# Optimization experiments

Measured on AMD Instinct MI355X. Metric: run time of the kernel, lower is better.

Reference implementation:

```python
import jax, jax.numpy as jnp
import numpy as np

N_NODES = 50000
N_EDGES = 800000
F_IN = 128
HIDDEN = 128
F_OUT = 64
BN_EPS = 1e-5


def setup_inputs() -> dict:
    key = jax.random.key(0)
    ks = jax.random.split(key, 8)
    features = jax.random.normal(ks[0], (N_NODES, F_IN), dtype=jnp.float32)
    W1 = jax.random.normal(ks[1], (2 * F_IN, HIDDEN), dtype=jnp.float32) * 0.05
    b1 = jnp.zeros((HIDDEN,), dtype=jnp.float32)
    gamma = jnp.ones((HIDDEN,), dtype=jnp.float32)
    beta = jnp.zeros((HIDDEN,), dtype=jnp.float32)
    W2 = jax.random.normal(ks[2], (2 * HIDDEN, F_OUT), dtype=jnp.float32) * 0.05
    b2 = jnp.zeros((F_OUT,), dtype=jnp.float32)
    edge_vals = jax.random.uniform(ks[3], (N_EDGES,), dtype=jnp.float32)
    edge_src = jax.random.randint(ks[4], (N_EDGES,), 0, N_NODES, dtype=jnp.int32)
    edge_dst = jax.random.randint(ks[5], (N_EDGES,), 0, N_NODES, dtype=jnp.int32)
    return {"features": features, "W1": W1, "b1": b1, "gamma": gamma,
            "beta": beta, "W2": W2, "b2": b2, "edge_vals": edge_vals,
            "edge_src": edge_src, "edge_dst": edge_dst}


def _spmm(edge_vals, edge_src, edge_dst, x):
    # agg[i] = sum_{e: dst_e == i} w_e * x[src_e]   (sparse adjacency @ x)
    msgs = edge_vals[:, None] * x[edge_src]          # [E, d]
    return jax.ops.segment_sum(msgs, edge_dst, num_segments=N_NODES)


def _batchnorm(x, gamma, beta):
    # BatchNorm1d in training mode: batch stats, biased variance
    mean = jnp.mean(x, axis=0)
    var = jnp.mean(jnp.square(x - mean), axis=0)
    return gamma * (x - mean) * jax.lax.rsqrt(var + BN_EPS) + beta


def reference(features, W1, b1, gamma, beta, W2, b2, edge_vals, edge_src, edge_dst):
    # Layer 1: SpMM -> concat -> linear -> batchnorm -> relu  (dropout is a no-op, p=0)
    agg = _spmm(edge_vals, edge_src, edge_dst, features)     # [N, F_IN]
    s = jnp.concatenate([agg, features], axis=1)             # [N, 2*F_IN]
    h = s @ W1 + b1                                          # [N, HIDDEN]
    h = jax.nn.relu(_batchnorm(h, gamma, beta))
    # Layer 2: SpMM -> concat -> linear (identity act, no norm)
    agg2 = _spmm(edge_vals, edge_src, edge_dst, h)           # [N, HIDDEN]
    s2 = jnp.concatenate([agg2, h], axis=1)                  # [N, 2*HIDDEN]
    out = s2 @ W2 + b2                                       # [N, F_OUT]
    return out
```

## Files before the change

### kernel.cpp

```cpp
#include <hip/hip_runtime.h>

#define N_NODES 50000
#define N_EDGES 800000
#define F_IN    128
#define HID     128
#define F_OUT   64
#define BN_EPS  1e-5f

#define NRANGES 196
#define NCHUNKS 196
#define CHUNK   4096
#define CVT_BLOCKS 3125
#define PREPW_BLOCKS 24

typedef __bf16 bf16x8 __attribute__((ext_vector_type(8)));
typedef float  f32x4  __attribute__((ext_vector_type(4)));

static inline size_t align_up(size_t x, size_t a){ return (x + a - 1) / a * a; }

__device__ __forceinline__ float bflo(unsigned u){ return __uint_as_float(u << 16); }
__device__ __forceinline__ float bfhi(unsigned u){ return __uint_as_float(u & 0xffff0000u); }
__device__ __forceinline__ unsigned packbf(float a, float b){
  __bf16 ha = (__bf16)a, hb = (__bf16)b;
  unsigned short ua = __builtin_bit_cast(unsigned short, ha);
  unsigned short ub = __builtin_bit_cast(unsigned short, hb);
  return (unsigned)ua | ((unsigned)ub << 16);
}


__global__ __launch_bounds__(256) void k_setup(
    const int* __restrict__ dst, const float* __restrict__ X,
    const float* __restrict__ W1, const float* __restrict__ W2,
    int* __restrict__ Hcr, __bf16* __restrict__ Sx,
    __bf16* __restrict__ W1f, __bf16* __restrict__ W2f,
    float* __restrict__ bn_acc, int* __restrict__ bar){
  __shared__ int hist[NRANGES];
  int b = blockIdx.x, t = threadIdx.x;
  if(b < NCHUNKS){
    if(t < NRANGES) hist[t] = 0;
    __syncthreads();
    int e0 = b * CHUNK;
    #pragma unroll
    for(int k = 0; k < CHUNK / 256; k++){
      int e = e0 + k * 256 + t;
      if(e < N_EDGES) atomicAdd(&hist[dst[e] >> 8], 1);
    }
    __syncthreads();
    if(t < NRANGES) Hcr[b * NRANGES + t] = hist[t];
  } else if(b < NCHUNKS + CVT_BLOCKS){
    int bb = b - NCHUNKS;
    if(bb == 0){
      bn_acc[t] = 0.f;
      if(t < 2) bar[t] = 0;
    }
    int idx = bb * 256 + t;
    int n = idx >> 4;
    int c = (idx & 15) * 8;
    const float* xp = X + (size_t)n * F_IN + c;
    f32x4 x0 = *(const f32x4*)xp;
    f32x4 x1 = *(const f32x4*)(xp + 4);
    bf16x8 v;
    #pragma unroll
    for(int i = 0; i < 4; i++){ v[i] = (__bf16)x0[i]; v[4 + i] = (__bf16)x1[i]; }
    *(bf16x8*)(Sx + (size_t)n * 128 + c) = v;
  } else {
    int s = (b - NCHUNKS - CVT_BLOCKS) * 256 + t;
    if(s < 4096){
      int ks = s >> 9, rem = s & 511, nf = rem >> 6, l = rem & 63;
      int k = ks * 32 + (l >> 4) * 8, c = nf * 16 + (l & 15);
      bf16x8 v;
      #pragma unroll
      for(int i = 0; i < 8; i++) v[i] = (__bf16)W1[(size_t)(k + i) * HID + c];
      *(bf16x8*)(W1f + ((size_t)s << 3)) = v;
    } else {
      int q = s - 4096;
      int ks = q >> 9, rem = q & 511, nf = rem >> 6, l = rem & 63;
      int k = ks * 32 + (l >> 4) * 8, c = nf * 16 + (l & 15);
      bf16x8 v;
      #pragma unroll
      for(int i = 0; i < 8; i++){
        int kk = k + i;
        float val = (c < 64) ? W2[(size_t)kk * F_OUT + c]
                             : W2[(size_t)(HID + kk) * F_OUT + (c - 64)];
        v[i] = (__bf16)val;
      }
      *(bf16x8*)(W2f + ((size_t)q << 3)) = v;
    }
  }
}


__device__ __forceinline__ void grid_bar(int* bar, int n){
  __syncthreads();
  if(threadIdx.x == 0){
    __threadfence();
    atomicAdd(bar, 1);
    while(atomicAdd(bar, 0) < n){ }
    __threadfence();
  }
  __syncthreads();
}

__global__ __launch_bounds__(256) void k_csr(
    const int* __restrict__ dst, const int* __restrict__ src, const float* __restrict__ vals,
    int* __restrict__ Hcr, int* __restrict__ rtot, int2* __restrict__ staged,
    unsigned* __restrict__ epack, int* __restrict__ rp, int* __restrict__ bar){
  __shared__ int s[256];
  __shared__ int aux[256];
  __shared__ int begS, endS;
  const int b = blockIdx.x, t = threadIdx.x;

  {
    int v = (t < NCHUNKS) ? Hcr[t * NRANGES + b] : 0;
    s[t] = v;
    __syncthreads();
    for(int off = 1; off < 256; off <<= 1){
      int u = (t >= off) ? s[t - off] : 0;
      __syncthreads();
      s[t] += u;
      __syncthreads();
    }
    if(t < NCHUNKS) Hcr[t * NRANGES + b] = s[t] - v;
    if(t == NCHUNKS - 1) rtot[b] = s[t];
  }
  grid_bar(&bar[0], NRANGES);

  {
    int tv = (t < NRANGES) ? rtot[t] : 0;
    s[t] = tv;
    __syncthreads();
    for(int off = 1; off < 256; off <<= 1){
      int u = (t >= off) ? s[t - off] : 0;
      __syncthreads();
      s[t] += u;
      __syncthreads();
    }
    if(t < NRANGES) aux[t] = (s[t] - tv) + Hcr[b * NRANGES + t];
    __syncthreads();
    int e0 = b * CHUNK;
    #pragma unroll
    for(int k = 0; k < CHUNK / 256; k++){
      int e = e0 + k * 256 + t;
      if(e < N_EDGES){
        int d = dst[e];
        int pos = atomicAdd(&aux[d >> 8], 1);
        staged[pos] = make_int2(__float_as_int(vals[e]), src[e] | ((d & 255) << 16));
      }
    }
  }
  grid_bar(&bar[1], NRANGES);

  {
    int tv = (t < NRANGES) ? rtot[t] : 0;
    s[t] = tv;
    __syncthreads();
    for(int off = 1; off < 256; off <<= 1){
      int u = (t >= off) ? s[t - off] : 0;
      __syncthreads();
      s[t] += u;
      __syncthreads();
    }
    if(t == b){ begS = s[t] - tv; endS = s[t]; }
    aux[t] = 0;
    __syncthreads();
    int beg = begS, end = endS;
    for(int i = beg + t; i < end; i += 256)
      atomicAdd(&aux[(staged[i].y >> 16) & 255], 1);
    __syncthreads();
    int v = aux[t];
    s[t] = v;
    __syncthreads();
    for(int off = 1; off < 256; off <<= 1){
      int u = (t >= off) ? s[t - off] : 0;
      __syncthreads();
      s[t] += u;
      __syncthreads();
    }
    int excl = s[t] - v;
    int d = b * 256 + t;
    if(d < N_NODES) rp[d] = beg + excl;
    if(b == NRANGES - 1 && t == 0) rp[N_NODES] = N_EDGES;
    __syncthreads();
    aux[t] = beg + excl;
    __syncthreads();
    for(int i = beg + t; i < end; i += 256){
      int2 e = staged[i];
      int dl = (e.y >> 16) & 255;
      int p = atomicAdd(&aux[dl], 1);
      unsigned wb = (unsigned)__builtin_bit_cast(unsigned short, (__bf16)__int_as_float(e.x));
      epack[p] = (wb << 16) | (unsigned)(e.y & 0xffff);
    }
  }
}


__global__ __launch_bounds__(256) void k_spmm1(const __bf16* __restrict__ Sx,
    __bf16* __restrict__ Sa, const unsigned* __restrict__ epack, const int* __restrict__ rp){
  int w    = (int)((blockIdx.x * blockDim.x + threadIdx.x) >> 6);
  int lane = threadIdx.x & 63;
  if(w >= N_NODES) return;
  int beg = rp[w], end = rp[w + 1];
  float a0 = 0.f, a1 = 0.f;
  int e = beg;
  for(; e + 7 < end; e += 8){
    unsigned q0 = epack[e],     q1 = epack[e + 1], q2 = epack[e + 2], q3 = epack[e + 3];
    unsigned q4 = epack[e + 4], q5 = epack[e + 5], q6 = epack[e + 6], q7 = epack[e + 7];
    unsigned u0 = *(const unsigned*)(Sx + (size_t)(q0 & 0xffff) * 128 + lane * 2);
    unsigned u1 = *(const unsigned*)(Sx + (size_t)(q1 & 0xffff) * 128 + lane * 2);
    unsigned u2 = *(const unsigned*)(Sx + (size_t)(q2 & 0xffff) * 128 + lane * 2);
    unsigned u3 = *(const unsigned*)(Sx + (size_t)(q3 & 0xffff) * 128 + lane * 2);
    unsigned u4 = *(const unsigned*)(Sx + (size_t)(q4 & 0xffff) * 128 + lane * 2);
    unsigned u5 = *(const unsigned*)(Sx + (size_t)(q5 & 0xffff) * 128 + lane * 2);
    unsigned u6 = *(const unsigned*)(Sx + (size_t)(q6 & 0xffff) * 128 + lane * 2);
    unsigned u7 = *(const unsigned*)(Sx + (size_t)(q7 & 0xffff) * 128 + lane * 2);
    float w0 = bfhi(q0), w1 = bfhi(q1), w2 = bfhi(q2), w3 = bfhi(q3);
    float w4 = bfhi(q4), w5 = bfhi(q5), w6 = bfhi(q6), w7 = bfhi(q7);
    a0 = fmaf(w0, bflo(u0), a0); a1 = fmaf(w0, bfhi(u0), a1);
    a0 = fmaf(w1, bflo(u1), a0); a1 = fmaf(w1, bfhi(u1), a1);
    a0 = fmaf(w2, bflo(u2), a0); a1 = fmaf(w2, bfhi(u2), a1);
    a0 = fmaf(w3, bflo(u3), a0); a1 = fmaf(w3, bfhi(u3), a1);
    a0 = fmaf(w4, bflo(u4), a0); a1 = fmaf(w4, bfhi(u4), a1);
    a0 = fmaf(w5, bflo(u5), a0); a1 = fmaf(w5, bfhi(u5), a1);
    a0 = fmaf(w6, bflo(u6), a0); a1 = fmaf(w6, bfhi(u6), a1);
    a0 = fmaf(w7, bflo(u7), a0); a1 = fmaf(w7, bfhi(u7), a1);
  }
  for(; e + 3 < end; e += 4){
    unsigned q0 = epack[e], q1 = epack[e + 1], q2 = epack[e + 2], q3 = epack[e + 3];
    unsigned u0 = *(const unsigned*)(Sx + (size_t)(q0 & 0xffff) * 128 + lane * 2);
    unsigned u1 = *(const unsigned*)(Sx + (size_t)(q1 & 0xffff) * 128 + lane * 2);
    unsigned u2 = *(const unsigned*)(Sx + (size_t)(q2 & 0xffff) * 128 + lane * 2);
    unsigned u3 = *(const unsigned*)(Sx + (size_t)(q3 & 0xffff) * 128 + lane * 2);
    float w0 = bfhi(q0), w1 = bfhi(q1), w2 = bfhi(q2), w3 = bfhi(q3);
    a0 = fmaf(w0, bflo(u0), a0); a1 = fmaf(w0, bfhi(u0), a1);
    a0 = fmaf(w1, bflo(u1), a0); a1 = fmaf(w1, bfhi(u1), a1);
    a0 = fmaf(w2, bflo(u2), a0); a1 = fmaf(w2, bfhi(u2), a1);
    a0 = fmaf(w3, bflo(u3), a0); a1 = fmaf(w3, bfhi(u3), a1);
  }
  for(; e < end; e++){
    unsigned q = epack[e];
    float wt = bfhi(q);
    unsigned u = *(const unsigned*)(Sx + (size_t)(q & 0xffff) * 128 + lane * 2);
    a0 = fmaf(wt, bflo(u), a0); a1 = fmaf(wt, bfhi(u), a1);
  }
  *(unsigned*)(Sa + (size_t)w * 128 + lane * 2) = packbf(a0, a1);
}


__global__ __launch_bounds__(256) void k_gemm1(
    const __bf16* __restrict__ Sa, const __bf16* __restrict__ Sx,
    const __bf16* __restrict__ W1f, const float* __restrict__ b1,
    __bf16* __restrict__ hpre, float* __restrict__ bn_acc){
  __shared__ float bnred[2][256];
  const int tid = threadIdx.x;
  const int lane = tid & 63, wid = tid >> 6;
  const int wm = wid >> 1, wn = wid & 1;
  const int lr = lane & 15, lk = (lane >> 4) * 8;
  const int rbase = blockIdx.x * 64 + wm * 32 + lr;

  f32x4 acc[2][4];
  #pragma unroll
  for(int m = 0; m < 2; m++)
    #pragma unroll
    for(int n = 0; n < 4; n++) acc[m][n] = (f32x4){0.f, 0.f, 0.f, 0.f};

  for(int ks = 0; ks < 8; ks++){
    const __bf16* src = (ks < 4) ? Sa : Sx;
    const int kb = (ks & 3) * 32 + lk;
    bf16x8 a[2], b[4];
    #pragma unroll
    for(int m = 0; m < 2; m++){
      int r = rbase + m * 16; if(r > N_NODES - 1) r = N_NODES - 1;
      a[m] = *(const bf16x8*)(src + (size_t)r * 128 + kb);
    }
    #pragma unroll
    for(int n = 0; n < 4; n++)
      b[n] = *(const bf16x8*)(W1f + (((ks * 8 + wn * 4 + n) * 64 + lane) << 3));
    #pragma unroll
    for(int m = 0; m < 2; m++)
      #pragma unroll
      for(int n = 0; n < 4; n++)
        acc[m][n] = __builtin_amdgcn_mfma_f32_16x16x32_bf16(a[m], b[n], acc[m][n], 0, 0, 0);
  }

  #pragma unroll
  for(int n = 0; n < 4; n++){
    int gc = wn * 64 + n * 16 + lr;
    float bias = b1[gc];
    float ps = 0.f, pq = 0.f;
    #pragma unroll
    for(int m = 0; m < 2; m++){
      int gr0 = blockIdx.x * 64 + wm * 32 + m * 16 + (lane >> 4) * 4;
      #pragma unroll
      for(int i = 0; i < 4; i++){
        int r = gr0 + i;
        if(r < N_NODES){
          float h = acc[m][n][i] + bias;
          hpre[(size_t)r * HID + gc] = (__bf16)h;
          ps += h; pq += h * h;
        }
      }
    }
    ps += __shfl_xor(ps, 16); ps += __shfl_xor(ps, 32);
    pq += __shfl_xor(pq, 16); pq += __shfl_xor(pq, 32);
    if(lane < 16){
      bnred[wm][gc] = ps;
      bnred[wm][128 + gc] = pq;
    }
  }
  __syncthreads();
  atomicAdd(&bn_acc[tid], bnred[0][tid] + bnred[1][tid]);
}


__global__ __launch_bounds__(256) void k_gemm2(
    const __bf16* __restrict__ hpre, const __bf16* __restrict__ W2f,
    const float* __restrict__ b2, const float* __restrict__ bn_acc,
    const float* __restrict__ gamma, const float* __restrict__ beta,
    __bf16* __restrict__ y2b, float* __restrict__ out){
  __shared__ float s_scale[HID], s_shift[HID];
  const int tid = threadIdx.x;
  if(tid < HID){
    float mean = bn_acc[tid] / (float)N_NODES;
    float var  = bn_acc[HID + tid] / (float)N_NODES - mean * mean;
    float rs   = rsqrtf(var + BN_EPS);
    float sc   = gamma[tid] * rs;
    s_scale[tid] = sc;
    s_shift[tid] = beta[tid] - mean * sc;
  }
  const int lane = tid & 63, wid = tid >> 6;
  const int wm = wid >> 1, wn = wid & 1;
  const int lr = lane & 15, lk = (lane >> 4) * 8;
  const int rbase = blockIdx.x * 64 + wm * 32 + lr;

  f32x4 acc[2][4];
  #pragma unroll
  for(int m = 0; m < 2; m++)
    #pragma unroll
    for(int n = 0; n < 4; n++) acc[m][n] = (f32x4){0.f, 0.f, 0.f, 0.f};
  __syncthreads();

  for(int ks = 0; ks < 4; ks++){
    int k0 = ks * 32 + lk;
    f32x4 sc0 = *(const f32x4*)(s_scale + k0);
    f32x4 sc1 = *(const f32x4*)(s_scale + k0 + 4);
    f32x4 sh0 = *(const f32x4*)(s_shift + k0);
    f32x4 sh1 = *(const f32x4*)(s_shift + k0 + 4);
    bf16x8 a[2], b[4];
    #pragma unroll
    for(int m = 0; m < 2; m++){
      int r = rbase + m * 16; if(r > N_NODES - 1) r = N_NODES - 1;
      bf16x8 hv = *(const bf16x8*)(hpre + (size_t)r * HID + k0);
      bf16x8 af;
      #pragma unroll
      for(int i = 0; i < 4; i++){
        af[i]     = (__bf16)fmaxf(0.f, fmaf((float)hv[i],     sc0[i], sh0[i]));
        af[4 + i] = (__bf16)fmaxf(0.f, fmaf((float)hv[4 + i], sc1[i], sh1[i]));
      }
      a[m] = af;
    }
    #pragma unroll
    for(int n = 0; n < 4; n++)
      b[n] = *(const bf16x8*)(W2f + (((ks * 8 + wn * 4 + n) * 64 + lane) << 3));
    #pragma unroll
    for(int m = 0; m < 2; m++)
      #pragma unroll
      for(int n = 0; n < 4; n++)
        acc[m][n] = __builtin_amdgcn_mfma_f32_16x16x32_bf16(a[m], b[n], acc[m][n], 0, 0, 0);
  }

  #pragma unroll
  for(int n = 0; n < 4; n++){
    int c = n * 16 + lr;
    float bias = (wn == 1) ? b2[c] : 0.f;
    #pragma unroll
    for(int m = 0; m < 2; m++){
      int gr0 = blockIdx.x * 64 + wm * 32 + m * 16 + (lane >> 4) * 4;
      #pragma unroll
      for(int i = 0; i < 4; i++){
        int r = gr0 + i;
        if(r < N_NODES){
          if(wn == 0) y2b[(size_t)r * F_OUT + c] = (__bf16)acc[m][n][i];
          else        out[(size_t)r * F_OUT + c] = acc[m][n][i] + bias;
        }
      }
    }
  }
}


__global__ __launch_bounds__(256) void k_spmm2(const __bf16* __restrict__ y2b,
    const unsigned* __restrict__ epack, const int* __restrict__ rp, float* __restrict__ out){
  int w    = (int)((blockIdx.x * blockDim.x + threadIdx.x) >> 6);
  int lane = threadIdx.x & 63;
  if(w >= N_NODES) return;
  int beg = rp[w], end = rp[w + 1];
  int half = lane >> 5, li = lane & 31;
  float a0 = 0.f, a1 = 0.f;
  int e = beg + half;
  for(; e + 6 < end; e += 8){
    unsigned q0 = epack[e],     q1 = epack[e + 2];
    unsigned q2 = epack[e + 4], q3 = epack[e + 6];
    unsigned u0 = *(const unsigned*)(y2b + (size_t)(q0 & 0xffff) * F_OUT + li * 2);
    unsigned u1 = *(const unsigned*)(y2b + (size_t)(q1 & 0xffff) * F_OUT + li * 2);
    unsigned u2 = *(const unsigned*)(y2b + (size_t)(q2 & 0xffff) * F_OUT + li * 2);
    unsigned u3 = *(const unsigned*)(y2b + (size_t)(q3 & 0xffff) * F_OUT + li * 2);
    float w0 = bfhi(q0), w1 = bfhi(q1), w2 = bfhi(q2), w3 = bfhi(q3);
    a0 = fmaf(w0, bflo(u0), a0); a1 = fmaf(w0, bfhi(u0), a1);
    a0 = fmaf(w1, bflo(u1), a0); a1 = fmaf(w1, bfhi(u1), a1);
    a0 = fmaf(w2, bflo(u2), a0); a1 = fmaf(w2, bfhi(u2), a1);
    a0 = fmaf(w3, bflo(u3), a0); a1 = fmaf(w3, bfhi(u3), a1);
  }
  for(; e < end; e += 2){
    unsigned q = epack[e];
    float wt = bfhi(q);
    unsigned u = *(const unsigned*)(y2b + (size_t)(q & 0xffff) * F_OUT + li * 2);
    a0 = fmaf(wt, bflo(u), a0); a1 = fmaf(wt, bfhi(u), a1);
  }
  a0 += __shfl_xor(a0, 32);
  a1 += __shfl_xor(a1, 32);
  if(lane < 32){
    float2 o = *(float2*)(out + (size_t)w * F_OUT + li * 2);
    o.x += a0; o.y += a1;
    *(float2*)(out + (size_t)w * F_OUT + li * 2) = o;
  }
}


extern "C" void kernel_launch(void* const* d_in, const int* in_sizes, int n_in,
                              void* d_out, int out_size, void* d_ws, size_t ws_size,
                              hipStream_t stream){
  const float* X     = (const float*)d_in[0];
  const float* W1    = (const float*)d_in[1];
  const float* b1    = (const float*)d_in[2];
  const float* gamma = (const float*)d_in[3];
  const float* beta  = (const float*)d_in[4];
  const float* W2    = (const float*)d_in[5];
  const float* b2    = (const float*)d_in[6];
  const float* evals = (const float*)d_in[7];
  const int*   esrc  = (const int*)d_in[8];
  const int*   edst  = (const int*)d_in[9];
  float* out = (float*)d_out;

  char* ws = (char*)d_ws;
  size_t off = 0;
  auto carve = [&](size_t bytes) -> char* {
    off = align_up(off, 256);
    char* p = ws + off;
    off += bytes;
    return p;
  };
  int*      Hcr    = (int*)     carve((size_t)NCHUNKS * NRANGES * 4);
  int*      rtot   = (int*)     carve((size_t)NRANGES * 4);
  int*      rp     = (int*)     carve(((size_t)N_NODES + 1) * 4);
  float*    bn_acc = (float*)   carve(256 * 4);
  int*      bar    = (int*)     carve(64 * 4);
  int2*     staged = (int2*)    carve((size_t)N_EDGES * 8);
  unsigned* epack  = (unsigned*)carve((size_t)N_EDGES * 4);
  __bf16*   W1f    = (__bf16*)  carve((size_t)4096 * 8 * 2);
  __bf16*   W2f    = (__bf16*)  carve((size_t)2048 * 8 * 2);
  __bf16*   Sa     = (__bf16*)  carve((size_t)N_NODES * 128 * 2);
  __bf16*   Sx     = (__bf16*)  carve((size_t)N_NODES * 128 * 2);
  __bf16*   hpre   = (__bf16*)  carve((size_t)N_NODES * HID * 2);
  __bf16*   y2b    = (__bf16*)  carve((size_t)N_NODES * F_OUT * 2);

  k_setup<<<NCHUNKS + CVT_BLOCKS + PREPW_BLOCKS, 256, 0, stream>>>(
      edst, X, W1, W2, Hcr, Sx, W1f, W2f, bn_acc, bar);
  k_csr<<<NRANGES, 256, 0, stream>>>(edst, esrc, evals, Hcr, rtot, staged, epack, rp, bar);

  k_spmm1<<<N_NODES / 4, 256, 0, stream>>>(Sx, Sa, epack, rp);
  k_gemm1<<<(N_NODES + 63) / 64, 256, 0, stream>>>(Sa, Sx, W1f, b1, hpre, bn_acc);
  k_gemm2<<<(N_NODES + 63) / 64, 256, 0, stream>>>(hpre, W2f, b2, bn_acc, gamma, beta, y2b, out);
  k_spmm2<<<N_NODES / 4, 256, 0, stream>>>(y2b, epack, rp, out);
}
```

Baseline: 259.4 us.

## Split persistent CSR kernel into three launches and unroll SpMM2 gather deeper

Replaces the single CSR-building kernel, which used spin-wait grid barriers on global atomics, with three separate kernel launches (range scan, scatter to staged, per-range local sort). Kernel boundaries now provide the ordering, which removes the barrier counters and their reset. The change trades spin-lock polling for two extra launch overheads. It also unrolls the layer-2 SpMM gather loop from 4 to 8 edges per half-wave, putting more loads in flight at the cost of more registers.

Measured after the change: 235.1 us. -9.4%, faster.

```diff
diff --git a/kernel.cpp b/kernel.cpp
--- a/kernel.cpp
+++ b/kernel.cpp
@@ -32,8 +32,7 @@
     const int* __restrict__ dst, const float* __restrict__ X,
     const float* __restrict__ W1, const float* __restrict__ W2,
     int* __restrict__ Hcr, __bf16* __restrict__ Sx,
-    __bf16* __restrict__ W1f, __bf16* __restrict__ W2f,
-    float* __restrict__ bn_acc, int* __restrict__ bar){
+    __bf16* __restrict__ W1f, __bf16* __restrict__ W2f, float* __restrict__ bn_acc){
   __shared__ int hist[NRANGES];
   int b = blockIdx.x, t = threadIdx.x;
   if(b < NCHUNKS){
@@ -49,10 +48,7 @@
     if(t < NRANGES) Hcr[b * NRANGES + t] = hist[t];
   } else if(b < NCHUNKS + CVT_BLOCKS){
     int bb = b - NCHUNKS;
-    if(bb == 0){
-      bn_acc[t] = 0.f;
-      if(t < 2) bar[t] = 0;
-    }
+    if(bb == 0) bn_acc[t] = 0.f;
     int idx = bb * 256 + t;
     int n = idx >> 4;
     int c = (idx & 15) * 8;
@@ -90,106 +86,97 @@
 }
 
 
-__device__ __forceinline__ void grid_bar(int* bar, int n){
-  __syncthreads();
-  if(threadIdx.x == 0){
-    __threadfence();
-    atomicAdd(bar, 1);
-    while(atomicAdd(bar, 0) < n){ }
-    __threadfence();
-  }
-  __syncthreads();
-}
-
-__global__ __launch_bounds__(256) void k_csr(
-    const int* __restrict__ dst, const int* __restrict__ src, const float* __restrict__ vals,
-    int* __restrict__ Hcr, int* __restrict__ rtot, int2* __restrict__ staged,
-    unsigned* __restrict__ epack, int* __restrict__ rp, int* __restrict__ bar){
+__global__ __launch_bounds__(256) void k_scanR(int* __restrict__ Hcr, int* __restrict__ rtot){
   __shared__ int s[256];
-  __shared__ int aux[256];
+  int r = blockIdx.x, t = threadIdx.x;
+  int v = (t < NCHUNKS) ? Hcr[t * NRANGES + r] : 0;
+  s[t] = v;
+  __syncthreads();
+  for(int off = 1; off < 256; off <<= 1){
+    int u = (t >= off) ? s[t - off] : 0;
+    __syncthreads();
+    s[t] += u;
+    __syncthreads();
+  }
+  if(t < NCHUNKS) Hcr[t * NRANGES + r] = s[t] - v;
+  if(t == NCHUNKS - 1) rtot[r] = s[t];
+}
+
+
+__global__ __launch_bounds__(256) void k_pass2(const int* __restrict__ dst, const int* __restrict__ src,
+    const float* __restrict__ vals, const int* __restrict__ Hcr,
+    const int* __restrict__ rtot, int2* __restrict__ staged){
+  __shared__ int s[256];
+  __shared__ int cur[NRANGES];
+  int c = blockIdx.x, t = threadIdx.x;
+  int tv = (t < NRANGES) ? rtot[t] : 0;
+  s[t] = tv;
+  __syncthreads();
+  for(int off = 1; off < 256; off <<= 1){
+    int u = (t >= off) ? s[t - off] : 0;
+    __syncthreads();
+    s[t] += u;
+    __syncthreads();
+  }
+  if(t < NRANGES) cur[t] = (s[t] - tv) + Hcr[c * NRANGES + t];
+  __syncthreads();
+  int e0 = c * CHUNK;
+  #pragma unroll
+  for(int k = 0; k < CHUNK / 256; k++){
+    int e = e0 + k * 256 + t;
+    if(e < N_EDGES){
+      int d = dst[e];
+      int pos = atomicAdd(&cur[d >> 8], 1);
+      staged[pos] = make_int2(__float_as_int(vals[e]), src[e] | ((d & 255) << 16));
+    }
+  }
+}
+
+
+__global__ __launch_bounds__(256) void k_pass3(const int2* __restrict__ staged,
+    const int* __restrict__ rtot, unsigned* __restrict__ epack, int* __restrict__ rp){
+  __shared__ int s[256];
+  __shared__ int cnt[256];
   __shared__ int begS, endS;
-  const int b = blockIdx.x, t = threadIdx.x;
-
-  {
-    int v = (t < NCHUNKS) ? Hcr[t * NRANGES + b] : 0;
-    s[t] = v;
-    __syncthreads();
-    for(int off = 1; off < 256; off <<= 1){
-      int u = (t >= off) ? s[t - off] : 0;
-      __syncthreads();
-      s[t] += u;
-      __syncthreads();
-    }
-    if(t < NCHUNKS) Hcr[t * NRANGES + b] = s[t] - v;
-    if(t == NCHUNKS - 1) rtot[b] = s[t];
-  }
-  grid_bar(&bar[0], NRANGES);
-
-  {
-    int tv = (t < NRANGES) ? rtot[t] : 0;
-    s[t] = tv;
-    __syncthreads();
-    for(int off = 1; off < 256; off <<= 1){
-      int u = (t >= off) ? s[t - off] : 0;
-      __syncthreads();
-      s[t] += u;
-      __syncthreads();
-    }
-    if(t < NRANGES) aux[t] = (s[t] - tv) + Hcr[b * NRANGES + t];
-    __syncthreads();
-    int e0 = b * CHUNK;
-    #pragma unroll
-    for(int k = 0; k < CHUNK / 256; k++){
-      int e = e0 + k * 256 + t;
-      if(e < N_EDGES){
-        int d = dst[e];
-        int pos = atomicAdd(&aux[d >> 8], 1);
-        staged[pos] = make_int2(__float_as_int(vals[e]), src[e] | ((d & 255) << 16));
-      }
-    }
-  }
-  grid_bar(&bar[1], NRANGES);
-
-  {
-    int tv = (t < NRANGES) ? rtot[t] : 0;
-    s[t] = tv;
-    __syncthreads();
-    for(int off = 1; off < 256; off <<= 1){
-      int u = (t >= off) ? s[t - off] : 0;
-      __syncthreads();
-      s[t] += u;
-      __syncthreads();
-    }
-    if(t == b){ begS = s[t] - tv; endS = s[t]; }
-    aux[t] = 0;
-    __syncthreads();
-    int beg = begS, end = endS;
-    for(int i = beg + t; i < end; i += 256)
-      atomicAdd(&aux[(staged[i].y >> 16) & 255], 1);
-    __syncthreads();
-    int v = aux[t];
-    s[t] = v;
-    __syncthreads();
-    for(int off = 1; off < 256; off <<= 1){
-      int u = (t >= off) ? s[t - off] : 0;
-      __syncthreads();
-      s[t] += u;
-      __syncthreads();
-    }
-    int excl = s[t] - v;
-    int d = b * 256 + t;
-    if(d < N_NODES) rp[d] = beg + excl;
-    if(b == NRANGES - 1 && t == 0) rp[N_NODES] = N_EDGES;
-    __syncthreads();
-    aux[t] = beg + excl;
-    __syncthreads();
-    for(int i = beg + t; i < end; i += 256){
-      int2 e = staged[i];
-      int dl = (e.y >> 16) & 255;
-      int p = atomicAdd(&aux[dl], 1);
-      unsigned wb = (unsigned)__builtin_bit_cast(unsigned short, (__bf16)__int_as_float(e.x));
-      epack[p] = (wb << 16) | (unsigned)(e.y & 0xffff);
-    }
+  int r = blockIdx.x, t = threadIdx.x;
+  int tv = (t < NRANGES) ? rtot[t] : 0;
+  s[t] = tv;
+  __syncthreads();
+  for(int off = 1; off < 256; off <<= 1){
+    int u = (t >= off) ? s[t - off] : 0;
+    __syncthreads();
+    s[t] += u;
+    __syncthreads();
+  }
+  if(t == r){ begS = s[t] - tv; endS = s[t]; }
+  cnt[t] = 0;
+  __syncthreads();
+  int beg = begS, end = endS;
+  for(int i = beg + t; i < end; i += 256)
+    atomicAdd(&cnt[(staged[i].y >> 16) & 255], 1);
+  __syncthreads();
+  int v = cnt[t];
+  s[t] = v;
+  __syncthreads();
+  for(int off = 1; off < 256; off <<= 1){
+    int u = (t >= off) ? s[t - off] : 0;
+    __syncthreads();
+    s[t] += u;
+    __syncthreads();
+  }
+  int excl = s[t] - v;
+  int d = r * 256 + t;
+  if(d < N_NODES) rp[d] = beg + excl;
+  if(r == NRANGES - 1 && t == 0) rp[N_NODES] = N_EDGES;
+  __syncthreads();
+  cnt[t] = beg + excl;
+  __syncthreads();
+  for(int i = beg + t; i < end; i += 256){
+    int2 e = staged[i];
+    int dl = (e.y >> 16) & 255;
+    int p = atomicAdd(&cnt[dl], 1);
+    unsigned wb = (unsigned)__builtin_bit_cast(unsigned short, (__bf16)__int_as_float(e.x));
+    epack[p] = (wb << 16) | (unsigned)(e.y & 0xffff);
   }
 }
 
@@ -397,18 +384,27 @@
   int half = lane >> 5, li = lane & 31;
   float a0 = 0.f, a1 = 0.f;
   int e = beg + half;
-  for(; e + 6 < end; e += 8){
-    unsigned q0 = epack[e],     q1 = epack[e + 2];
-    unsigned q2 = epack[e + 4], q3 = epack[e + 6];
+  for(; e + 14 < end; e += 16){
+    unsigned q0 = epack[e],      q1 = epack[e + 2],  q2 = epack[e + 4],  q3 = epack[e + 6];
+    unsigned q4 = epack[e + 8],  q5 = epack[e + 10], q6 = epack[e + 12], q7 = epack[e + 14];
     unsigned u0 = *(const unsigned*)(y2b + (size_t)(q0 & 0xffff) * F_OUT + li * 2);
     unsigned u1 = *(const unsigned*)(y2b + (size_t)(q1 & 0xffff) * F_OUT + li * 2);
     unsigned u2 = *(const unsigned*)(y2b + (size_t)(q2 & 0xffff) * F_OUT + li * 2);
     unsigned u3 = *(const unsigned*)(y2b + (size_t)(q3 & 0xffff) * F_OUT + li * 2);
+    unsigned u4 = *(const unsigned*)(y2b + (size_t)(q4 & 0xffff) * F_OUT + li * 2);
+    unsigned u5 = *(const unsigned*)(y2b + (size_t)(q5 & 0xffff) * F_OUT + li * 2);
+    unsigned u6 = *(const unsigned*)(y2b + (size_t)(q6 & 0xffff) * F_OUT + li * 2);
+    unsigned u7 = *(const unsigned*)(y2b + (size_t)(q7 & 0xffff) * F_OUT + li * 2);
     float w0 = bfhi(q0), w1 = bfhi(q1), w2 = bfhi(q2), w3 = bfhi(q3);
+    float w4 = bfhi(q4), w5 = bfhi(q5), w6 = bfhi(q6), w7 = bfhi(q7);
     a0 = fmaf(w0, bflo(u0), a0); a1 = fmaf(w0, bfhi(u0), a1);
     a0 = fmaf(w1, bflo(u1), a0); a1 = fmaf(w1, bfhi(u1), a1);
     a0 = fmaf(w2, bflo(u2), a0); a1 = fmaf(w2, bfhi(u2), a1);
     a0 = fmaf(w3, bflo(u3), a0); a1 = fmaf(w3, bfhi(u3), a1);
+    a0 = fmaf(w4, bflo(u4), a0); a1 = fmaf(w4, bfhi(u4), a1);
+    a0 = fmaf(w5, bflo(u5), a0); a1 = fmaf(w5, bfhi(u5), a1);
+    a0 = fmaf(w6, bflo(u6), a0); a1 = fmaf(w6, bfhi(u6), a1);
+    a0 = fmaf(w7, bflo(u7), a0); a1 = fmaf(w7, bfhi(u7), a1);
   }
   for(; e < end; e += 2){
     unsigned q = epack[e];
@@ -453,7 +449,6 @@
   int*      rtot   = (int*)     carve((size_t)NRANGES * 4);
   int*      rp     = (int*)     carve(((size_t)N_NODES + 1) * 4);
   float*    bn_acc = (float*)   carve(256 * 4);
-  int*      bar    = (int*)     carve(64 * 4);
   int2*     staged = (int2*)    carve((size_t)N_EDGES * 8);
   unsigned* epack  = (unsigned*)carve((size_t)N_EDGES * 4);
   __bf16*   W1f    = (__bf16*)  carve((size_t)4096 * 8 * 2);
@@ -464,8 +459,10 @@
   __bf16*   y2b    = (__bf16*)  carve((size_t)N_NODES * F_OUT * 2);
 
   k_setup<<<NCHUNKS + CVT_BLOCKS + PREPW_BLOCKS, 256, 0, stream>>>(
-      edst, X, W1, W2, Hcr, Sx, W1f, W2f, bn_acc, bar);
-  k_csr<<<NRANGES, 256, 0, stream>>>(edst, esrc, evals, Hcr, rtot, staged, epack, rp, bar);
+      edst, X, W1, W2, Hcr, Sx, W1f, W2f, bn_acc);
+  k_scanR<<<NRANGES, 256, 0, stream>>>(Hcr, rtot);
+  k_pass2<<<NCHUNKS, 256, 0, stream>>>(edst, esrc, evals, Hcr, rtot, staged);
+  k_pass3<<<NRANGES, 256, 0, stream>>>(staged, rtot, epack, rp);
 
   k_spmm1<<<N_NODES / 4, 256, 0, stream>>>(Sx, Sa, epack, rp);
   k_gemm1<<<(N_NODES + 63) / 64, 256, 0, stream>>>(Sa, Sx, W1f, b1, hpre, bn_acc);
```
